# Kernel optimization log

Hardware: AMD Instinct MI355X
Metric: run time of the kernel (lower is better)

The kernel has to match this reference:

```python
import jax, jax.numpy as jnp
import numpy as np

N = 100000   # nodes
E = 2500000  # edges (before self-loops)
G = 64       # graphs in the batch


def _glorot(key, fi, fo):
    return jax.random.normal(key, (fi, fo), jnp.float32) * jnp.sqrt(2.0 / (fi + fo))


def setup_inputs() -> dict:
    key = jax.random.key(0)
    ks = jax.random.split(key, 8)
    x = jax.random.normal(ks[0], (N, 3), jnp.float32)
    edge_index = jax.random.randint(ks[1], (2, E), 0, N)
    batch = jnp.sort(jax.random.randint(ks[2], (N,), 0, G))
    return dict(
        x=x, edge_index=edge_index, batch=batch,
        W1=_glorot(ks[3], 3, 16),  b1=jnp.zeros((16,), jnp.float32),
        W2=_glorot(ks[4], 16, 32), b2=jnp.zeros((32,), jnp.float32),
        W3=_glorot(ks[5], 32, 16), b3=jnp.zeros((16,), jnp.float32),
        W4=_glorot(ks[6], 16, 2),  b4=jnp.zeros((2,), jnp.float32),
    )


def reference(x, edge_index, batch, W1, b1, W2, b2, W3, b3, W4, b4):
    # PyG GCNConv: add self-loops, sym-normalize by deg^{-1/2}, gather->scatter-add.
    loops = jnp.arange(N)
    src = jnp.concatenate([edge_index[0], loops])  # [E+N]
    dst = jnp.concatenate([edge_index[1], loops])
    deg = jax.ops.segment_sum(jnp.ones_like(dst, jnp.float32), dst, num_segments=N)
    dinv = jax.lax.rsqrt(jnp.maximum(deg, 1.0))  # deg >= 1 due to self-loops
    norm = (dinv[src] * dinv[dst])[:, None]      # [E+N, 1]

    def gcn_conv(h, W, b):
        h = h @ W                                  # [N, out]
        msg = h[src] * norm                        # gather + edge scaling
        agg = jax.ops.segment_sum(msg, dst, num_segments=N)  # scatter-add
        return agg + b

    h = jax.nn.relu(gcn_conv(x, W1, b1))
    h = jax.nn.relu(gcn_conv(h, W2, b2))
    h = jax.nn.relu(gcn_conv(h, W3, b3))
    # F.dropout with training=False (module in eval) is identity
    h = gcn_conv(h, W4, b4)                        # [N, 2]

    # global_mean_pool over graph ids
    sums = jax.ops.segment_sum(h, batch, num_segments=G)
    cnts = jax.ops.segment_sum(jnp.ones((N,), h.dtype), batch, num_segments=G)
    pooled = sums / jnp.maximum(cnts, 1.0)[:, None]  # [G, 2]
    return jax.nn.log_softmax(pooled, axis=1)
```

## Files before the change

### kernel.cpp

```cpp
#include <hip/hip_runtime.h>
#include <hip/hip_fp16.h>
#include <cmath>

static constexpr int NN = 100000;
static constexpr int NE = 2500000;
static constexpr int NG = 64;
static constexpr int NBUCK = (NN + 255) / 256;
static constexpr int CHUNK = 4096;
static constexpr int NCHUNK = (NE + CHUNK - 1) / CHUNK;
static constexpr int CAP = 8192;

union H8 { float4 f4; __half2 h2[4]; };
union H4 { float2 f2; __half2 h2[2]; };

__device__ inline void unpack_add(float* a, float4 r) {
    H8 u; u.f4 = r;
#pragma unroll
    for (int k = 0; k < 4; ++k) { float2 f = __half22float2(u.h2[k]); a[2*k] += f.x; a[2*k+1] += f.y; }
}
__device__ inline unsigned pack2(float f0, float f1) {
    __half2 h = __floats2half2_rn(f0, f1);
    return *reinterpret_cast<unsigned*>(&h);
}

__global__ void p1_hist(const int* __restrict__ dst, int* __restrict__ Ht) {
    __shared__ int hist[NBUCK];
    int t = threadIdx.x, c = blockIdx.x;
    for (int i = t; i < NBUCK; i += 256) hist[i] = 0;
    __syncthreads();
    int e0 = c * CHUNK, e1 = min(e0 + CHUNK, NE);
    for (int e = e0 + t; e < e1; e += 256) atomicAdd(&hist[dst[e] >> 8], 1);
    __syncthreads();
    for (int b = t; b < NBUCK; b += 256) Ht[(size_t)b * NCHUNK + c] = hist[b];
}

__global__ void p2_scan(int* __restrict__ Ht, int* __restrict__ count,
                        float* __restrict__ pooled3) {
    __shared__ int s[256];
    int b = blockIdx.x, t = threadIdx.x;
    if (b == 0 && t < NG * 3) pooled3[t] = 0.0f;
    int* row = Ht + (size_t)b * NCHUNK;
    int carry = 0;
    for (int seg = 0; seg < 3; ++seg) {
        int idx = seg * 256 + t;
        int v = (idx < NCHUNK) ? row[idx] : 0;
        __syncthreads();
        s[t] = v;
        __syncthreads();
#pragma unroll
        for (int off = 1; off < 256; off <<= 1) {
            int y = (t >= off) ? s[t - off] : 0;
            __syncthreads();
            s[t] += y;
            __syncthreads();
        }
        int incl = s[t];
        int segtot = s[255];
        if (idx < NCHUNK) row[idx] = incl - v + carry;
        carry += segtot;
    }
    if (t == 0) count[b] = carry;
}

__global__ void p3_scatter(const int* __restrict__ src, const int* __restrict__ dst,
                           const int* __restrict__ Ht, int* __restrict__ staging) {
    __shared__ int cur[NBUCK];
    int t = threadIdx.x, bid = blockIdx.x;
    int x = bid & 7, o = bid >> 3;
    int len = 76 + (x < 3 ? 1 : 0);
    if (o >= len) return;
    int c = x * 76 + min(x, 3) + o;
    for (int b = t; b < NBUCK; b += 256) cur[b] = Ht[(size_t)b * NCHUNK + c];
    __syncthreads();
    int e0 = c * CHUNK, e1 = min(e0 + CHUNK, NE);
    for (int e = e0 + t; e < e1; e += 256) {
        int d = dst[e];
        int b = d >> 8;
        int r = atomicAdd(&cur[b], 1);
        staging[((size_t)b << 13) + r] = src[e] | ((d & 255) << 17);
    }
}

__global__ void csr_build_kernel(const int* __restrict__ staging, const int* __restrict__ count,
                                 const float* __restrict__ x,
                                 int* __restrict__ deg_i, float* __restrict__ dinv,
                                 int* __restrict__ row_start, int* __restrict__ csr_src,
                                 float2* __restrict__ xsh) {
    __shared__ int hist[256];
    __shared__ int scn[256];
    __shared__ int cur[256];
    int b = blockIdx.x, t = threadIdx.x;
    int cnt = count[b];
    int base = b << 13;
    hist[t] = 0;
    __syncthreads();
    const int* st = staging + ((size_t)b << 13);
    for (int i = t; i < cnt; i += 256) atomicAdd(&hist[st[i] >> 17], 1);
    __syncthreads();
    int h = hist[t];
    scn[t] = h; __syncthreads();
#pragma unroll
    for (int off = 1; off < 256; off <<= 1) {
        int y = (t >= off) ? scn[t - off] : 0;
        __syncthreads();
        scn[t] += y;
        __syncthreads();
    }
    int ex = scn[t] - h;
    int v = (b << 8) + t;
    if (v < NN) {
        float dv = rsqrtf((float)h + 1.0f);
        deg_i[v]     = h;
        row_start[v] = base + ex;
        dinv[v]      = dv;
        H4 u;
        u.h2[0] = __floats2half2_rn(x[v * 3] * dv, x[v * 3 + 1] * dv);
        u.h2[1] = __floats2half2_rn(x[v * 3 + 2] * dv, 0.0f);
        xsh[v] = u.f2;
    }
    cur[t] = ex;
    __syncthreads();
    for (int i = t; i < cnt; i += 256) {
        int p = st[i];
        int r = atomicAdd(&cur[p >> 17], 1);
        csr_src[base + r] = p & 0x1FFFF;
    }
}

__global__ void __launch_bounds__(256) agg3t1_kernel(const float2* __restrict__ xsh,
        const int* __restrict__ csr, const int* __restrict__ rs, const int* __restrict__ deg,
        const float* __restrict__ dinv, const float* __restrict__ W1,
        const float* __restrict__ b1, unsigned* __restrict__ g2h) {
    __shared__ float sW1[48], sb1[16];
    int t = threadIdx.x;
    if (t < 48) sW1[t] = W1[t];
    if (t < 16) sb1[t] = b1[t];
    __syncthreads();
    int tid = blockIdx.x * 256 + t;
    int v = tid >> 3, p = tid & 7;
    if (v >= NN) return;
    float a0 = 0.0f, a1 = 0.0f, a2 = 0.0f;
    if (p == 0) {
        H4 u; u.f2 = xsh[v];
        float2 f0 = __half22float2(u.h2[0]), f1 = __half22float2(u.h2[1]);
        a0 = f0.x; a1 = f0.y; a2 = f1.x;
    }
    int s0 = rs[v], cnt = deg[v];
    for (int j = p; j < cnt; j += 8) {
        H4 u; u.f2 = xsh[csr[s0 + j]];
        float2 f0 = __half22float2(u.h2[0]), f1 = __half22float2(u.h2[1]);
        a0 += f0.x; a1 += f0.y; a2 += f1.x;
    }
    a0 += __shfl_xor(a0, 1); a1 += __shfl_xor(a1, 1); a2 += __shfl_xor(a2, 1);
    a0 += __shfl_xor(a0, 2); a1 += __shfl_xor(a1, 2); a2 += __shfl_xor(a2, 2);
    a0 += __shfl_xor(a0, 4); a1 += __shfl_xor(a1, 4); a2 += __shfl_xor(a2, 4);
    float dv = dinv[v];
    a0 *= dv; a1 *= dv; a2 *= dv;
    float f[2];
#pragma unroll
    for (int k = 0; k < 2; ++k) {
        int fo = p * 2 + k;
        float g = fmaf(a0, sW1[fo], fmaf(a1, sW1[16 + fo], fmaf(a2, sW1[32 + fo], sb1[fo])));
        f[k] = fmaxf(g, 0.0f) * dv;
    }
    g2h[v * 8 + p] = pack2(f[0], f[1]);
}

__global__ void __launch_bounds__(256) agg16mid_kernel(const float4* __restrict__ g2h,
        const int* __restrict__ csr, const int* __restrict__ rs, const int* __restrict__ deg,
        const float* __restrict__ dinv, const float* __restrict__ W2,
        const float* __restrict__ b2, const float* __restrict__ W3,
        unsigned* __restrict__ g3h) {
    __shared__ float sW2[512], sW3[512], sb2[32];
    int t = threadIdx.x;
    for (int i = t; i < 512; i += 256) { sW2[i] = W2[i]; sW3[i] = W3[i]; }
    if (t < 32) sb2[t] = b2[t];
    __syncthreads();
    int tid = blockIdx.x * 256 + t;
    int v = tid >> 3, p = tid & 7;
    if (v >= NN) return;
    float a[16];
#pragma unroll
    for (int f = 0; f < 16; ++f) a[f] = 0.0f;
    if (p == 0) { unpack_add(a, g2h[v * 2]); unpack_add(a + 8, g2h[v * 2 + 1]); }
    int s0 = rs[v], cnt = deg[v];
    for (int j = p; j < cnt; j += 8) {
        int s = csr[s0 + j];
        unpack_add(a,     g2h[s * 2]);
        unpack_add(a + 8, g2h[s * 2 + 1]);
    }
#pragma unroll
    for (int f = 0; f < 16; ++f) a[f] += __shfl_xor(a[f], 1);
#pragma unroll
    for (int f = 0; f < 16; ++f) a[f] += __shfl_xor(a[f], 2);
#pragma unroll
    for (int f = 0; f < 16; ++f) a[f] += __shfl_xor(a[f], 4);
    float dv = dinv[v];
#pragma unroll
    for (int f = 0; f < 16; ++f) a[f] *= dv;
    float h2[32];
#pragma unroll
    for (int fo = 0; fo < 32; ++fo) {
        float s = sb2[fo];
#pragma unroll
        for (int fi = 0; fi < 16; ++fi) s = fmaf(a[fi], sW2[fi * 32 + fo], s);
        h2[fo] = fmaxf(s, 0.0f);
    }
    float o[2];
#pragma unroll
    for (int k = 0; k < 2; ++k) {
        int fo = p * 2 + k;
        float s = 0.0f;
#pragma unroll
        for (int fi = 0; fi < 32; ++fi) s = fmaf(h2[fi], sW3[fi * 16 + fo], s);
        o[k] = s * dv;
    }
    g3h[v * 8 + p] = pack2(o[0], o[1]);
}

__global__ void __launch_bounds__(256) agg16t4_kernel(const float4* __restrict__ g3h,
        const int* __restrict__ csr, const int* __restrict__ rs, const int* __restrict__ deg,
        const float* __restrict__ dinv, const float* __restrict__ b3,
        const float* __restrict__ W4, float2* __restrict__ g4) {
    __shared__ float sb3[16], sW4[32];
    int t = threadIdx.x;
    if (t < 16) sb3[t] = b3[t];
    if (t < 32) sW4[t] = W4[t];
    __syncthreads();
    int tid = blockIdx.x * 256 + t;
    int v = tid >> 3, p = tid & 7;
    if (v >= NN) return;
    float a[16];
#pragma unroll
    for (int f = 0; f < 16; ++f) a[f] = 0.0f;
    if (p == 0) { unpack_add(a, g3h[v * 2]); unpack_add(a + 8, g3h[v * 2 + 1]); }
    int s0 = rs[v], cnt = deg[v];
    for (int j = p; j < cnt; j += 8) {
        int s = csr[s0 + j];
        unpack_add(a,     g3h[s * 2]);
        unpack_add(a + 8, g3h[s * 2 + 1]);
    }
#pragma unroll
    for (int f = 0; f < 16; ++f) a[f] += __shfl_xor(a[f], 1);
#pragma unroll
    for (int f = 0; f < 16; ++f) a[f] += __shfl_xor(a[f], 2);
#pragma unroll
    for (int f = 0; f < 16; ++f) a[f] += __shfl_xor(a[f], 4);
    if (p != 0) return;
    float dv = dinv[v];
    float o0 = 0.0f, o1 = 0.0f;
#pragma unroll
    for (int f = 0; f < 16; ++f) {
        float h3 = fmaxf(fmaf(a[f], dv, sb3[f]), 0.0f);
        o0 = fmaf(h3, sW4[f * 2 + 0], o0);
        o1 = fmaf(h3, sW4[f * 2 + 1], o1);
    }
    g4[v] = make_float2(o0 * dv, o1 * dv);
}

__global__ void __launch_bounds__(256) agg2pool_kernel(const float2* __restrict__ g4,
        const int* __restrict__ csr, const int* __restrict__ rs, const int* __restrict__ deg,
        const float* __restrict__ dinv, const float* __restrict__ b4,
        const int* __restrict__ batch, float* __restrict__ pooled3) {
    __shared__ float spool[NG * 3];
    int t = threadIdx.x;
    for (int i = t; i < NG * 3; i += 256) spool[i] = 0.0f;
    __syncthreads();
    int tid = blockIdx.x * 256 + t;
    int v = tid >> 3, p = tid & 7;
    if (v < NN) {
        float a0 = 0.0f, a1 = 0.0f;
        if (p == 0) { float2 s = g4[v]; a0 = s.x; a1 = s.y; }
        int s0 = rs[v], cnt = deg[v];
        for (int j = p; j < cnt; j += 8) {
            float2 q = g4[csr[s0 + j]];
            a0 += q.x; a1 += q.y;
        }
        a0 += __shfl_xor(a0, 1); a1 += __shfl_xor(a1, 1);
        a0 += __shfl_xor(a0, 2); a1 += __shfl_xor(a1, 2);
        a0 += __shfl_xor(a0, 4); a1 += __shfl_xor(a1, 4);
        if (p == 0) {
            float dv = dinv[v];
            float o0 = fmaf(a0, dv, b4[0]);
            float o1 = fmaf(a1, dv, b4[1]);
            int gi = batch[v];
            atomicAdd(&spool[gi * 3 + 0], o0);
            atomicAdd(&spool[gi * 3 + 1], o1);
            atomicAdd(&spool[gi * 3 + 2], 1.0f);
        }
    }
    __syncthreads();
    for (int i = t; i < NG * 3; i += 256)
        if (spool[i] != 0.0f) atomicAdd(&pooled3[i], spool[i]);
}

__global__ void lsm_kernel(const float* __restrict__ pooled3, float* __restrict__ out) {
    int g = threadIdx.x;
    if (g < NG) {
        float c = fmaxf(pooled3[g * 3 + 2], 1.0f);
        float a = pooled3[g * 3 + 0] / c;
        float b = pooled3[g * 3 + 1] / c;
        float m = fmaxf(a, b);
        float lse = m + logf(expf(a - m) + expf(b - m));
        out[g * 2 + 0] = a - lse;
        out[g * 2 + 1] = b - lse;
    }
}

extern "C" void kernel_launch(void* const* d_in, const int* in_sizes, int n_in,
                              void* d_out, int out_size, void* d_ws, size_t ws_size,
                              hipStream_t stream) {
    (void)in_sizes; (void)n_in; (void)out_size; (void)ws_size;

    const float* x   = (const float*)d_in[0];
    const int*   ei  = (const int*)d_in[1];
    const int*   bat = (const int*)d_in[2];
    const float* W1  = (const float*)d_in[3];
    const float* b1  = (const float*)d_in[4];
    const float* W2  = (const float*)d_in[5];
    const float* b2  = (const float*)d_in[6];
    const float* W3  = (const float*)d_in[7];
    const float* b3  = (const float*)d_in[8];
    const float* W4  = (const float*)d_in[9];
    const float* b4  = (const float*)d_in[10];
    float* out = (float*)d_out;

    const int* src = ei;
    const int* dst = ei + NE;

    char* w = (char*)d_ws;
    int*      Ht        = (int*)w;      w += ((size_t)NBUCK * NCHUNK * 4 + 15) & ~15ull;
    int*      count     = (int*)w;      w += ((size_t)NBUCK * 4 + 15) & ~15ull;
    int*      staging   = (int*)w;      w += (size_t)NBUCK * CAP * 4;
    int*      csr_src   = (int*)w;      w += (size_t)NBUCK * CAP * 4;
    int*      deg_i     = (int*)w;      w += (size_t)NN * 4;
    int*      row_start = (int*)w;      w += (size_t)NN * 4;
    float*    dinv      = (float*)w;    w += (size_t)NN * 4;
    float2*   xsh       = (float2*)w;   w += (size_t)NN * 8;
    unsigned* g2h       = (unsigned*)w; w += (size_t)NN * 32;
    unsigned* g3h       = (unsigned*)w; w += (size_t)NN * 32;
    float2*   g4        = (float2*)w;   w += (size_t)NN * 8;
    float*    pooled3   = (float*)w;    w += NG * 3 * 4;

    const int gN8 = (NN * 8 + 255) / 256;

    p1_hist<<<NCHUNK, 256, 0, stream>>>(dst, Ht);
    p2_scan<<<NBUCK, 256, 0, stream>>>(Ht, count, pooled3);
    p3_scatter<<<616, 256, 0, stream>>>(src, dst, Ht, staging);
    csr_build_kernel<<<NBUCK, 256, 0, stream>>>(staging, count, x, deg_i, dinv, row_start,
                                                csr_src, xsh);

    agg3t1_kernel<<<gN8, 256, 0, stream>>>(xsh, csr_src, row_start, deg_i, dinv, W1, b1, g2h);
    agg16mid_kernel<<<gN8, 256, 0, stream>>>((const float4*)g2h, csr_src, row_start, deg_i,
                                             dinv, W2, b2, W3, g3h);
    agg16t4_kernel<<<gN8, 256, 0, stream>>>((const float4*)g3h, csr_src, row_start, deg_i,
                                            dinv, b3, W4, g4);
    agg2pool_kernel<<<gN8, 256, 0, stream>>>(g4, csr_src, row_start, deg_i, dinv, b4, bat,
                                             pooled3);

    lsm_kernel<<<1, 64, 0, stream>>>(pooled3, out);
}
```

Measured before the change: 158.2 us.

## Pack row start and degree into one word; split dense layer math across lanes

Row start and degree are packed into a single 32-bit word (23 bits of offset, 9 bits of degree), so each aggregation kernel does one index load per node instead of two. In the middle layer, each of the 8 lanes per node now computes 4 of the 32 hidden features and a partial 16-wide product, then combines them with shuffles. Before, every lane computed all 32 hidden features redundantly. The last-layer projection is likewise split across lanes with a shuffle reduction. This cuts redundant FMAs and register pressure but adds shuffles, and it assumes node degree stays below 512.

```diff
diff --git a/kernel.cpp b/kernel.cpp
--- a/kernel.cpp
+++ b/kernel.cpp
@@ -83,9 +83,8 @@
 
 __global__ void csr_build_kernel(const int* __restrict__ staging, const int* __restrict__ count,
                                  const float* __restrict__ x,
-                                 int* __restrict__ deg_i, float* __restrict__ dinv,
-                                 int* __restrict__ row_start, int* __restrict__ csr_src,
-                                 float2* __restrict__ xsh) {
+                                 unsigned* __restrict__ rsd, float* __restrict__ dinv,
+                                 int* __restrict__ csr_src, float2* __restrict__ xsh) {
     __shared__ int hist[256];
     __shared__ int scn[256];
     __shared__ int cur[256];
@@ -110,9 +109,8 @@
     int v = (b << 8) + t;
     if (v < NN) {
         float dv = rsqrtf((float)h + 1.0f);
-        deg_i[v]     = h;
-        row_start[v] = base + ex;
-        dinv[v]      = dv;
+        rsd[v]  = (unsigned)(base + ex) | ((unsigned)h << 23);
+        dinv[v] = dv;
         H4 u;
         u.h2[0] = __floats2half2_rn(x[v * 3] * dv, x[v * 3 + 1] * dv);
         u.h2[1] = __floats2half2_rn(x[v * 3 + 2] * dv, 0.0f);
@@ -128,7 +126,7 @@
 }
 
 __global__ void __launch_bounds__(256) agg3t1_kernel(const float2* __restrict__ xsh,
-        const int* __restrict__ csr, const int* __restrict__ rs, const int* __restrict__ deg,
+        const int* __restrict__ csr, const unsigned* __restrict__ rsd,
         const float* __restrict__ dinv, const float* __restrict__ W1,
         const float* __restrict__ b1, unsigned* __restrict__ g2h) {
     __shared__ float sW1[48], sb1[16];
@@ -145,7 +143,8 @@
         float2 f0 = __half22float2(u.h2[0]), f1 = __half22float2(u.h2[1]);
         a0 = f0.x; a1 = f0.y; a2 = f1.x;
     }
-    int s0 = rs[v], cnt = deg[v];
+    unsigned rd = rsd[v];
+    int s0 = rd & 0x7FFFFF, cnt = rd >> 23;
     for (int j = p; j < cnt; j += 8) {
         H4 u; u.f2 = xsh[csr[s0 + j]];
         float2 f0 = __half22float2(u.h2[0]), f1 = __half22float2(u.h2[1]);
@@ -167,7 +166,7 @@
 }
 
 __global__ void __launch_bounds__(256) agg16mid_kernel(const float4* __restrict__ g2h,
-        const int* __restrict__ csr, const int* __restrict__ rs, const int* __restrict__ deg,
+        const int* __restrict__ csr, const unsigned* __restrict__ rsd,
         const float* __restrict__ dinv, const float* __restrict__ W2,
         const float* __restrict__ b2, const float* __restrict__ W3,
         unsigned* __restrict__ g3h) {
@@ -183,7 +182,8 @@
 #pragma unroll
     for (int f = 0; f < 16; ++f) a[f] = 0.0f;
     if (p == 0) { unpack_add(a, g2h[v * 2]); unpack_add(a + 8, g2h[v * 2 + 1]); }
-    int s0 = rs[v], cnt = deg[v];
+    unsigned rd = rsd[v];
+    int s0 = rd & 0x7FFFFF, cnt = rd >> 23;
     for (int j = p; j < cnt; j += 8) {
         int s = csr[s0 + j];
         unpack_add(a,     g2h[s * 2]);
@@ -198,28 +198,35 @@
     float dv = dinv[v];
 #pragma unroll
     for (int f = 0; f < 16; ++f) a[f] *= dv;
-    float h2[32];
-#pragma unroll
-    for (int fo = 0; fo < 32; ++fo) {
+    float h2p[4];
+#pragma unroll
+    for (int k = 0; k < 4; ++k) {
+        int fo = p * 4 + k;
         float s = sb2[fo];
 #pragma unroll
         for (int fi = 0; fi < 16; ++fi) s = fmaf(a[fi], sW2[fi * 32 + fo], s);
-        h2[fo] = fmaxf(s, 0.0f);
-    }
-    float o[2];
-#pragma unroll
-    for (int k = 0; k < 2; ++k) {
-        int fo = p * 2 + k;
-        float s = 0.0f;
-#pragma unroll
-        for (int fi = 0; fi < 32; ++fi) s = fmaf(h2[fi], sW3[fi * 16 + fo], s);
-        o[k] = s * dv;
-    }
-    g3h[v * 8 + p] = pack2(o[0], o[1]);
+        h2p[k] = fmaxf(s, 0.0f);
+    }
+    float po[16];
+#pragma unroll
+    for (int fo = 0; fo < 16; ++fo) {
+        float s = h2p[0] * sW3[(p * 4 + 0) * 16 + fo];
+        s = fmaf(h2p[1], sW3[(p * 4 + 1) * 16 + fo], s);
+        s = fmaf(h2p[2], sW3[(p * 4 + 2) * 16 + fo], s);
+        s = fmaf(h2p[3], sW3[(p * 4 + 3) * 16 + fo], s);
+        po[fo] = s;
+    }
+#pragma unroll
+    for (int f = 0; f < 16; ++f) po[f] += __shfl_xor(po[f], 1);
+#pragma unroll
+    for (int f = 0; f < 16; ++f) po[f] += __shfl_xor(po[f], 2);
+#pragma unroll
+    for (int f = 0; f < 16; ++f) po[f] += __shfl_xor(po[f], 4);
+    g3h[v * 8 + p] = pack2(po[p * 2] * dv, po[p * 2 + 1] * dv);
 }
 
 __global__ void __launch_bounds__(256) agg16t4_kernel(const float4* __restrict__ g3h,
-        const int* __restrict__ csr, const int* __restrict__ rs, const int* __restrict__ deg,
+        const int* __restrict__ csr, const unsigned* __restrict__ rsd,
         const float* __restrict__ dinv, const float* __restrict__ b3,
         const float* __restrict__ W4, float2* __restrict__ g4) {
     __shared__ float sb3[16], sW4[32];
@@ -234,7 +241,8 @@
 #pragma unroll
     for (int f = 0; f < 16; ++f) a[f] = 0.0f;
     if (p == 0) { unpack_add(a, g3h[v * 2]); unpack_add(a + 8, g3h[v * 2 + 1]); }
-    int s0 = rs[v], cnt = deg[v];
+    unsigned rd = rsd[v];
+    int s0 = rd & 0x7FFFFF, cnt = rd >> 23;
     for (int j = p; j < cnt; j += 8) {
         int s = csr[s0 + j];
         unpack_add(a,     g3h[s * 2]);
@@ -246,20 +254,20 @@
     for (int f = 0; f < 16; ++f) a[f] += __shfl_xor(a[f], 2);
 #pragma unroll
     for (int f = 0; f < 16; ++f) a[f] += __shfl_xor(a[f], 4);
-    if (p != 0) return;
     float dv = dinv[v];
-    float o0 = 0.0f, o1 = 0.0f;
-#pragma unroll
-    for (int f = 0; f < 16; ++f) {
-        float h3 = fmaxf(fmaf(a[f], dv, sb3[f]), 0.0f);
-        o0 = fmaf(h3, sW4[f * 2 + 0], o0);
-        o1 = fmaf(h3, sW4[f * 2 + 1], o1);
-    }
-    g4[v] = make_float2(o0 * dv, o1 * dv);
+    int f0 = p * 2, f1 = p * 2 + 1;
+    float h3a = fmaxf(fmaf(a[f0], dv, sb3[f0]), 0.0f);
+    float h3b = fmaxf(fmaf(a[f1], dv, sb3[f1]), 0.0f);
+    float o0 = fmaf(h3a, sW4[f0 * 2 + 0], h3b * sW4[f1 * 2 + 0]);
+    float o1 = fmaf(h3a, sW4[f0 * 2 + 1], h3b * sW4[f1 * 2 + 1]);
+    o0 += __shfl_xor(o0, 1); o1 += __shfl_xor(o1, 1);
+    o0 += __shfl_xor(o0, 2); o1 += __shfl_xor(o1, 2);
+    o0 += __shfl_xor(o0, 4); o1 += __shfl_xor(o1, 4);
+    if (p == 0) g4[v] = make_float2(o0 * dv, o1 * dv);
 }
 
 __global__ void __launch_bounds__(256) agg2pool_kernel(const float2* __restrict__ g4,
-        const int* __restrict__ csr, const int* __restrict__ rs, const int* __restrict__ deg,
+        const int* __restrict__ csr, const unsigned* __restrict__ rsd,
         const float* __restrict__ dinv, const float* __restrict__ b4,
         const int* __restrict__ batch, float* __restrict__ pooled3) {
     __shared__ float spool[NG * 3];
@@ -271,7 +279,8 @@
     if (v < NN) {
         float a0 = 0.0f, a1 = 0.0f;
         if (p == 0) { float2 s = g4[v]; a0 = s.x; a1 = s.y; }
-        int s0 = rs[v], cnt = deg[v];
+        unsigned rd = rsd[v];
+        int s0 = rd & 0x7FFFFF, cnt = rd >> 23;
         for (int j = p; j < cnt; j += 8) {
             float2 q = g4[csr[s0 + j]];
             a0 += q.x; a1 += q.y;
@@ -329,34 +338,30 @@
     const int* dst = ei + NE;
 
     char* w = (char*)d_ws;
-    int*      Ht        = (int*)w;      w += ((size_t)NBUCK * NCHUNK * 4 + 15) & ~15ull;
-    int*      count     = (int*)w;      w += ((size_t)NBUCK * 4 + 15) & ~15ull;
-    int*      staging   = (int*)w;      w += (size_t)NBUCK * CAP * 4;
-    int*      csr_src   = (int*)w;      w += (size_t)NBUCK * CAP * 4;
-    int*      deg_i     = (int*)w;      w += (size_t)NN * 4;
-    int*      row_start = (int*)w;      w += (size_t)NN * 4;
-    float*    dinv      = (float*)w;    w += (size_t)NN * 4;
-    float2*   xsh       = (float2*)w;   w += (size_t)NN * 8;
-    unsigned* g2h       = (unsigned*)w; w += (size_t)NN * 32;
-    unsigned* g3h       = (unsigned*)w; w += (size_t)NN * 32;
-    float2*   g4        = (float2*)w;   w += (size_t)NN * 8;
-    float*    pooled3   = (float*)w;    w += NG * 3 * 4;
+    int*      Ht      = (int*)w;      w += ((size_t)NBUCK * NCHUNK * 4 + 15) & ~15ull;
+    int*      count   = (int*)w;      w += ((size_t)NBUCK * 4 + 15) & ~15ull;
+    int*      staging = (int*)w;      w += (size_t)NBUCK * CAP * 4;
+    int*      csr_src = (int*)w;      w += (size_t)NBUCK * CAP * 4;
+    unsigned* rsd     = (unsigned*)w; w += (size_t)NN * 4;
+    float*    dinv    = (float*)w;    w += (size_t)NN * 4;
+    float2*   xsh     = (float2*)w;   w += (size_t)NN * 8;
+    unsigned* g2h     = (unsigned*)w; w += (size_t)NN * 32;
+    unsigned* g3h     = (unsigned*)w; w += (size_t)NN * 32;
+    float2*   g4      = (float2*)w;   w += (size_t)NN * 8;
+    float*    pooled3 = (float*)w;    w += NG * 3 * 4;
 
     const int gN8 = (NN * 8 + 255) / 256;
 
     p1_hist<<<NCHUNK, 256, 0, stream>>>(dst, Ht);
     p2_scan<<<NBUCK, 256, 0, stream>>>(Ht, count, pooled3);
     p3_scatter<<<616, 256, 0, stream>>>(src, dst, Ht, staging);
-    csr_build_kernel<<<NBUCK, 256, 0, stream>>>(staging, count, x, deg_i, dinv, row_start,
-                                                csr_src, xsh);
-
-    agg3t1_kernel<<<gN8, 256, 0, stream>>>(xsh, csr_src, row_start, deg_i, dinv, W1, b1, g2h);
-    agg16mid_kernel<<<gN8, 256, 0, stream>>>((const float4*)g2h, csr_src, row_start, deg_i,
-                                             dinv, W2, b2, W3, g3h);
-    agg16t4_kernel<<<gN8, 256, 0, stream>>>((const float4*)g3h, csr_src, row_start, deg_i,
-                                            dinv, b3, W4, g4);
-    agg2pool_kernel<<<gN8, 256, 0, stream>>>(g4, csr_src, row_start, deg_i, dinv, b4, bat,
-                                             pooled3);
+    csr_build_kernel<<<NBUCK, 256, 0, stream>>>(staging, count, x, rsd, dinv, csr_src, xsh);
+
+    agg3t1_kernel<<<gN8, 256, 0, stream>>>(xsh, csr_src, rsd, dinv, W1, b1, g2h);
+    agg16mid_kernel<<<gN8, 256, 0, stream>>>((const float4*)g2h, csr_src, rsd, dinv, W2, b2,
+                                             W3, g3h);
+    agg16t4_kernel<<<gN8, 256, 0, stream>>>((const float4*)g3h, csr_src, rsd, dinv, b3, W4, g4);
+    agg2pool_kernel<<<gN8, 256, 0, stream>>>(g4, csr_src, rsd, dinv, b4, bat, pooled3);
 
     lsm_kernel<<<1, 64, 0, stream>>>(pooled3, out);
 }
```

Measured after the change: 162.4 us. 2.6% more time.
